# Performance work log

Measured on AMD Instinct MI355X. Metric: run time of the kernel, lower is better.

The kernel has to match this reference:

```python
import jax, jax.numpy as jnp
import numpy as np

EPS = 1e-05
BITW = 8
BITA = 8


def _ste_round(v):
    # round with identity gradient (TF Round->Identity override)
    return v + jax.lax.stop_gradient(jnp.round(v) - v)


def _quantize_overflow(x, bits):
    # tensorlayer _quantize_overflow: linear quantization over [min, max]
    n = 2.0 ** bits - 1.0
    mx = jnp.max(x)
    mn = jnp.min(x)
    step = jax.lax.stop_gradient((mx - mn) / n)
    return _ste_round((x - mn) / step) * step + mn


def _conv2d_same(x, w):
    # x: [N,H,W,C], w: [KH,KW,C,F]
    return jax.lax.conv_general_dilated(
        x, w, window_strides=(1, 1), padding='SAME',
        dimension_numbers=('NHWC', 'HWIO', 'NHWC'))


def setup_inputs() -> dict:
    key = jax.random.key(0)
    k1, k2 = jax.random.split(key)
    x = jax.random.normal(k1, (32, 56, 56, 128), dtype=jnp.float32)
    W = jax.random.normal(k2, (3, 3, 128, 256), dtype=jnp.float32) * 0.02
    gamma = jnp.ones((256,), dtype=jnp.float32)
    beta = jnp.zeros((256,), dtype=jnp.float32)
    return {"x": x, "W": W, "gamma": gamma, "beta": beta}


def reference(x, W, gamma, beta):
    # 1) fake-quantize activations
    xq = _quantize_overflow(x, BITA)
    # 2) full-precision conv to get batch statistics (training path)
    conv_out = _conv2d_same(x, W)  # [N,H,W,F]
    mean = jnp.mean(conv_out, axis=(0, 1, 2))          # [F]
    var = jnp.var(conv_out, axis=(0, 1, 2))            # [F], biased (tf.nn.moments)
    inv_std = 1.0 / jnp.sqrt(var + EPS)                # [F]
    # 3) fold BN into weights/bias
    w_fold = W * (gamma * inv_std)                     # broadcast over [KH,KW,C,F]
    bias_fold = beta - gamma * mean * inv_std          # [F]
    # 4) quantize folded weights, conv with quantized activations
    wq = _quantize_overflow(w_fold, BITW)
    out = _conv2d_same(xq, wq) + bias_fold
    return jax.nn.relu(out)
```

## Files before the change

kernel.cpp:

```cpp
#include <hip/hip_runtime.h>

typedef float f32x4_t __attribute__((ext_vector_type(4)));
typedef __bf16 bf16x8_t __attribute__((ext_vector_type(8)));
typedef unsigned short u16x8_t __attribute__((ext_vector_type(8)));

#define NPIX        100352
#define PIX_PER_IMG 3136
#define PH          58
#define PPIX        3364
#define C_IN        128
#define C_OUT       256
#define NTAPS       9
#define NV4         3211264
#define NWELEM      294912
#define MBLK        784
#define NPADPIX     107648

#define OFF_ENC     0
#define OFF_WQP     16
#define OFF_XQP     32
#define OFF_SCALE   64
#define OFF_BIAS    1152
#define OFF_WT      4096
#define OFF_WQT     593920
#define OFF_PSUM    1183744
#define OFF_PSQ     1986560
#define OFF_XPAD    2789376
#define OFF_XQPAD   30347264

__device__ __forceinline__ unsigned short f2bf(float x) {
  unsigned u = __float_as_uint(x);
  u += 0x7FFFu + ((u >> 16) & 1u);
  return (unsigned short)(u >> 16);
}
__device__ __forceinline__ unsigned encf(float v) {
  unsigned u = __float_as_uint(v);
  return (u & 0x80000000u) ? ~u : (u | 0x80000000u);
}
__device__ __forceinline__ float decf(unsigned e) {
  unsigned u = (e & 0x80000000u) ? (e ^ 0x80000000u) : ~e;
  return __uint_as_float(u);
}
__device__ __forceinline__ void gl_lds16(const void* g, void* l) {
  auto gp = (const __attribute__((address_space(1))) unsigned*)(const unsigned*)g;
  auto lp = (__attribute__((address_space(3))) unsigned*)(unsigned*)l;
  __builtin_amdgcn_global_load_lds(gp, lp, 16, 0, 0);
}

__global__ void kinit(unsigned* enc) {
  enc[0] = 0xFFFFFFFFu;
  enc[1] = 0u;
  enc[2] = 0xFFFFFFFFu;
  enc[3] = 0u;
}

__global__ void kminmax(const float4* __restrict__ x, unsigned* __restrict__ enc) {
  const int tid = blockIdx.x * blockDim.x + threadIdx.x;
  const int stride = gridDim.x * blockDim.x;
  float mn = 3.4e38f, mx = -3.4e38f;
  for (int i = tid; i < NV4; i += stride) {
    float4 v = x[i];
    mn = fminf(mn, fminf(fminf(v.x, v.y), fminf(v.z, v.w)));
    mx = fmaxf(mx, fmaxf(fmaxf(v.x, v.y), fmaxf(v.z, v.w)));
  }
  #pragma unroll
  for (int off = 32; off > 0; off >>= 1) {
    mn = fminf(mn, __shfl_xor(mn, off));
    mx = fmaxf(mx, __shfl_xor(mx, off));
  }
  __shared__ float smn[4], smx[4];
  const int lane = threadIdx.x & 63, w = threadIdx.x >> 6;
  if (lane == 0) { smn[w] = mn; smx[w] = mx; }
  __syncthreads();
  if (threadIdx.x == 0) {
    mn = fminf(fminf(smn[0], smn[1]), fminf(smn[2], smn[3]));
    mx = fmaxf(fmaxf(smx[0], smx[1]), fmaxf(smx[2], smx[3]));
    atomicMin(&enc[0], encf(mn));
    atomicMax(&enc[1], encf(mx));
  }
}

__global__ void kprep(const unsigned* __restrict__ enc, float* __restrict__ xqp) {
  const float mn = decf(enc[0]), mx = decf(enc[1]);
  xqp[0] = mn;
  xqp[1] = (mx - mn) / 255.0f;
  xqp[2] = 255.0f / (mx - mn);
}

__global__ void kwconv(const float* __restrict__ W, unsigned short* __restrict__ wt) {
  const int idx = blockIdx.x * 256 + threadIdx.x;
  if (idx >= NWELEM) return;
  const int c = idx & 127;
  const int f = (idx >> 7) & 255;
  const int tap = idx >> 15;
  wt[idx] = f2bf(W[(tap * 128 + c) * 256 + f]);
}

__global__ void kwq(const float* __restrict__ W, const float* __restrict__ scale,
                    const float* __restrict__ wqp, unsigned short* __restrict__ wqt) {
  const int idx = blockIdx.x * 256 + threadIdx.x;
  if (idx >= NWELEM) return;
  const int c = idx & 127;
  const int f = (idx >> 7) & 255;
  const int tap = idx >> 15;
  const float wmn = wqp[0], wstep = wqp[1], wrstep = wqp[2];
  const float v = W[(tap * 128 + c) * 256 + f] * scale[f];
  const float q = rintf((v - wmn) * wrstep) * wstep + wmn;
  wqt[idx] = f2bf(q);
}

__global__ void kpadfill(const float* __restrict__ x, const float* __restrict__ xqp,
                         unsigned short* __restrict__ xpad, unsigned short* __restrict__ xqpad)
{
  const int tid = blockIdx.x * 256 + threadIdx.x;
  if (tid >= NPADPIX * 16) return;
  const int pp = tid >> 4;
  const int c8 = (tid & 15) << 3;
  const int n = pp / PPIX;
  const int rem = pp - n * PPIX;
  const int hp = rem / PH;
  const int wp = rem - hp * PH;
  u16x8_t vb, vq;
  #pragma unroll
  for (int j = 0; j < 8; ++j) { vb[j] = 0; vq[j] = 0; }
  if (hp >= 1 && hp <= 56 && wp >= 1 && wp <= 56) {
    const float mn = xqp[0], step = xqp[1], rstep = xqp[2];
    const float* src = x + ((n * PIX_PER_IMG) + (hp - 1) * 56 + (wp - 1)) * C_IN + c8;
    const float4 a = *(const float4*)src;
    const float4 b = *(const float4*)(src + 4);
    const float v[8] = {a.x, a.y, a.z, a.w, b.x, b.y, b.z, b.w};
    #pragma unroll
    for (int j = 0; j < 8; ++j) {
      vb[j] = f2bf(v[j]);
      const float qv = rintf((v[j] - mn) * rstep) * step + mn;
      vq[j] = f2bf(qv);
    }
  }
  *(u16x8_t*)(xpad + pp * C_IN + c8) = vb;
  *(u16x8_t*)(xqpad + pp * C_IN + c8) = vq;
}

template<int STATS>
__global__ __launch_bounds__(512, 4)
void kconv(const unsigned short* __restrict__ xin,
           const unsigned short* __restrict__ wt,
           float* __restrict__ out,
           const float* __restrict__ bias,
           float* __restrict__ psum,
           float* __restrict__ psq)
{
  const int bm = blockIdx.x;
  const int bn = blockIdx.y;
  const int tid = threadIdx.x;
  const int lane = tid & 63;
  const int wid = tid >> 6;
  const int wm = wid >> 2;
  const int wn = wid & 3;
  const int l16 = lane & 15;
  const int rsub = lane >> 4;

  __shared__ __align__(16) unsigned char smem[65536];
  unsigned char* smA = smem;
  unsigned char* smB = smem + 32768;

  const int rbase = wid * 4 + rsub;
  const int gchunk = (l16 & 8) | ((l16 & 7) ^ (rbase & 7));

  unsigned aoff[4];
  #pragma unroll
  for (int i = 0; i < 4; ++i) {
    const int pix = bm * 128 + i * 32 + rbase;
    const int n = pix / PIX_PER_IMG;
    const int rem = pix - n * PIX_PER_IMG;
    const int h = rem / 56;
    const int w = rem - h * 56;
    aoff[i] = (unsigned)((n * PPIX + h * PH + w) * C_IN + gchunk * 8);
  }
  unsigned boff[4];
  #pragma unroll
  for (int i = 0; i < 4; ++i) {
    const int f = bn * 128 + i * 32 + rbase;
    boff[i] = (unsigned)(f * C_IN + gchunk * 8);
  }

  f32x4_t acc[4][2];
  #pragma unroll
  for (int im = 0; im < 4; ++im)
    #pragma unroll
    for (int in = 0; in < 2; ++in)
      #pragma unroll
      for (int k = 0; k < 4; ++k) acc[im][in][k] = 0.f;

  #pragma unroll 1
  for (int tap = 0; tap < NTAPS; ++tap) {
    const int kh = tap / 3, kw = tap - kh * 3;
    const unsigned atap = (unsigned)((kh * PH + kw) * C_IN);
    const unsigned btap = (unsigned)(tap * C_OUT * C_IN);
    __syncthreads();
    #pragma unroll
    for (int i = 0; i < 4; ++i)
      gl_lds16(xin + atap + aoff[i], smA + i * 8192 + wid * 1024);
    #pragma unroll
    for (int i = 0; i < 4; ++i)
      gl_lds16(wt + btap + boff[i], smB + i * 8192 + wid * 1024);
    __syncthreads();

    #pragma unroll
    for (int kb = 0; kb < 4; ++kb) {
      bf16x8_t av[4], bv[2];
      const int c = kb * 4 + rsub;
      const int p = (c & 8) | ((c & 7) ^ (l16 & 7));
      #pragma unroll
      for (int im = 0; im < 4; ++im) {
        const int row = wm * 64 + im * 16 + l16;
        av[im] = *(const bf16x8_t*)(smA + row * 256 + p * 16);
      }
      #pragma unroll
      for (int in = 0; in < 2; ++in) {
        const int row = wn * 32 + in * 16 + l16;
        bv[in] = *(const bf16x8_t*)(smB + row * 256 + p * 16);
      }
      #pragma unroll
      for (int im = 0; im < 4; ++im)
        #pragma unroll
        for (int in = 0; in < 2; ++in)
          acc[im][in] = __builtin_amdgcn_mfma_f32_16x16x32_bf16(av[im], bv[in], acc[im][in], 0, 0, 0);
    }
  }

  if (STATS) {
    __syncthreads();
    float* sb = (float*)smem;
    #pragma unroll
    for (int in = 0; in < 2; ++in) {
      float s = 0.f, q = 0.f;
      #pragma unroll
      for (int im = 0; im < 4; ++im)
        #pragma unroll
        for (int j = 0; j < 4; ++j) {
          const float v = acc[im][in][j];
          s += v; q += v * v;
        }
      s += __shfl_xor(s, 16); q += __shfl_xor(q, 16);
      s += __shfl_xor(s, 32); q += __shfl_xor(q, 32);
      if (lane < 16) {
        sb[wid * 32 + in * 16 + lane] = s;
        sb[256 + wid * 32 + in * 16 + lane] = q;
      }
    }
    __syncthreads();
    if (tid < 128) {
      const int wn2 = tid >> 5, cw = tid & 31;
      const float s = sb[wn2 * 32 + cw] + sb[(4 + wn2) * 32 + cw];
      const float q = sb[256 + wn2 * 32 + cw] + sb[256 + (4 + wn2) * 32 + cw];
      const int b = bm * 2 + bn;
      psum[b * 128 + tid] = s;
      psq[b * 128 + tid] = q;
    }
  } else {
    float bval[2];
    #pragma unroll
    for (int in = 0; in < 2; ++in)
      bval[in] = bias[bn * 128 + wn * 32 + in * 16 + l16];
    #pragma unroll
    for (int im = 0; im < 4; ++im) {
      #pragma unroll
      for (int j = 0; j < 4; ++j) {
        const int pix = bm * 128 + wm * 64 + im * 16 + rsub * 4 + j;
        #pragma unroll
        for (int in = 0; in < 2; ++in) {
          const int f = bn * 128 + wn * 32 + in * 16 + l16;
          out[pix * 256 + f] = fmaxf(acc[im][in][j] + bval[in], 0.f);
        }
      }
    }
  }
}

__global__ __launch_bounds__(256)
void kstats(const float* __restrict__ psum, const float* __restrict__ psq,
            const float* __restrict__ gamma, const float* __restrict__ beta,
            float* __restrict__ scale, float* __restrict__ bias)
{
  const int ch = blockIdx.x;
  const int bn = ch >> 7, col = ch & 127;
  float s = 0.f, q = 0.f;
  for (int bm = threadIdx.x; bm < MBLK; bm += 256) {
    const int b = bm * 2 + bn;
    s += psum[b * 128 + col];
    q += psq[b * 128 + col];
  }
  #pragma unroll
  for (int off = 32; off > 0; off >>= 1) {
    s += __shfl_xor(s, off);
    q += __shfl_xor(q, off);
  }
  __shared__ float ss[4], sq2[4];
  const int lane = threadIdx.x & 63, w = threadIdx.x >> 6;
  if (lane == 0) { ss[w] = s; sq2[w] = q; }
  __syncthreads();
  if (threadIdx.x == 0) {
    s = ss[0] + ss[1] + ss[2] + ss[3];
    q = sq2[0] + sq2[1] + sq2[2] + sq2[3];
    const float inv = 1.0f / (float)NPIX;
    const float mean = s * inv;
    const float var = q * inv - mean * mean;
    const float istd = 1.0f / sqrtf(var + 1e-5f);
    const float g = gamma[ch];
    scale[ch] = g * istd;
    bias[ch] = beta[ch] - g * mean * istd;
  }
}

__global__ __launch_bounds__(256)
void kwmm(const float* __restrict__ W, const float* __restrict__ scale,
          unsigned* __restrict__ enc)
{
  const int idx = blockIdx.x * 256 + threadIdx.x;
  float v = 0.f;
  if (idx < NWELEM) v = W[idx] * scale[idx & 255];
  float mn = v, mx = v;
  #pragma unroll
  for (int off = 32; off > 0; off >>= 1) {
    mn = fminf(mn, __shfl_xor(mn, off));
    mx = fmaxf(mx, __shfl_xor(mx, off));
  }
  __shared__ float rmn[4], rmx[4];
  const int lane = threadIdx.x & 63, w = threadIdx.x >> 6;
  if (lane == 0) { rmn[w] = mn; rmx[w] = mx; }
  __syncthreads();
  if (threadIdx.x == 0) {
    mn = fminf(fminf(rmn[0], rmn[1]), fminf(rmn[2], rmn[3]));
    mx = fmaxf(fmaxf(rmx[0], rmx[1]), fmaxf(rmx[2], rmx[3]));
    atomicMin(&enc[2], encf(mn));
    atomicMax(&enc[3], encf(mx));
  }
}

__global__ void kwprep(const unsigned* __restrict__ enc, float* __restrict__ wqp) {
  const float mn = decf(enc[2]), mx = decf(enc[3]);
  wqp[0] = mn;
  wqp[1] = (mx - mn) / 255.0f;
  wqp[2] = 255.0f / (mx - mn);
}

extern "C" void kernel_launch(void* const* d_in, const int* in_sizes, int n_in,
                              void* d_out, int out_size, void* d_ws, size_t ws_size,
                              hipStream_t stream)
{
  const float* x     = (const float*)d_in[0];
  const float* W     = (const float*)d_in[1];
  const float* gamma = (const float*)d_in[2];
  const float* beta  = (const float*)d_in[3];
  float* out = (float*)d_out;
  char* ws = (char*)d_ws;

  unsigned* enc        = (unsigned*)(ws + OFF_ENC);
  float* wqp           = (float*)(ws + OFF_WQP);
  float* xqp           = (float*)(ws + OFF_XQP);
  float* scale         = (float*)(ws + OFF_SCALE);
  float* bias          = (float*)(ws + OFF_BIAS);
  unsigned short* Wt   = (unsigned short*)(ws + OFF_WT);
  unsigned short* Wqt  = (unsigned short*)(ws + OFF_WQT);
  float* psum          = (float*)(ws + OFF_PSUM);
  float* psq           = (float*)(ws + OFF_PSQ);
  unsigned short* xpad  = (unsigned short*)(ws + OFF_XPAD);
  unsigned short* xqpad = (unsigned short*)(ws + OFF_XQPAD);

  kinit<<<1, 64, 0, stream>>>(enc);
  kminmax<<<1024, 256, 0, stream>>>((const float4*)x, enc);
  kprep<<<1, 64, 0, stream>>>(enc, xqp);
  kwconv<<<1152, 256, 0, stream>>>(W, Wt);
  kpadfill<<<6728, 256, 0, stream>>>(x, xqp, xpad, xqpad);
  kconv<1><<<dim3(MBLK, 2), 512, 0, stream>>>(xpad, Wt, nullptr, nullptr, psum, psq);
  kstats<<<256, 256, 0, stream>>>(psum, psq, gamma, beta, scale, bias);
  kwmm<<<1152, 256, 0, stream>>>(W, scale, enc);
  kwprep<<<1, 64, 0, stream>>>(enc, wqp);
  kwq<<<1152, 256, 0, stream>>>(W, scale, wqp, Wqt);
  kconv<0><<<dim3(MBLK, 2), 512, 0, stream>>>(xqpad, Wqt, out, bias, nullptr, nullptr);
}
```

Baseline: 257.9 us.

## Enlarge conv tiles to 256x128, double-buffer half-tap K stages, remap blocks per XCD

The implicit-GEMM conv kernel now computes 256-pixel by 128-filter tiles per block, with each warp holding a 64x64 accumulator (16 MFMA tiles). The K loop is split into 18 half-tap stages of 64 channels and double-buffered in 96KB of LDS, so the next stage's global-to-LDS load overlaps the MFMAs of the current one. Blocks are remapped so that each XCD gets a contiguous range of pixel tiles, which should improve L2 reuse. In exchange, register and LDS pressure rise (launch bounds drop to 2 blocks per CU), and the stats partials are indexed for the new tile shape.

```diff
diff --git a/kernel.cpp b/kernel.cpp
--- a/kernel.cpp
+++ b/kernel.cpp
@@ -13,7 +13,7 @@
 #define NTAPS       9
 #define NV4         3211264
 #define NWELEM      294912
-#define MBLK        784
+#define MBLK2       392
 #define NPADPIX     107648
 
 #define OFF_ENC     0
@@ -141,7 +141,7 @@
 }
 
 template<int STATS>
-__global__ __launch_bounds__(512, 4)
+__global__ __launch_bounds__(512, 2)
 void kconv(const unsigned short* __restrict__ xin,
            const unsigned short* __restrict__ wt,
            float* __restrict__ out,
@@ -149,90 +149,97 @@
            float* __restrict__ psum,
            float* __restrict__ psq)
 {
-  const int bm = blockIdx.x;
-  const int bn = blockIdx.y;
+  const int l = blockIdx.x;
+  const int xcd = l & 7, k = l >> 3;
+  const int bn = k & 1;
+  const int bm = xcd * 49 + (k >> 1);
+
   const int tid = threadIdx.x;
   const int lane = tid & 63;
   const int wid = tid >> 6;
-  const int wm = wid >> 2;
-  const int wn = wid & 3;
+  const int wm = wid >> 1;
+  const int wn = wid & 1;
   const int l16 = lane & 15;
   const int rsub = lane >> 4;
 
-  __shared__ __align__(16) unsigned char smem[65536];
-  unsigned char* smA = smem;
-  unsigned char* smB = smem + 32768;
-
-  const int rbase = wid * 4 + rsub;
-  const int gchunk = (l16 & 8) | ((l16 & 7) ^ (rbase & 7));
-
+  __shared__ __align__(16) unsigned char smem[98304];
+
+  const int lrow = lane >> 3;
+  const int lchunk = (lane & 7) ^ lrow;
   unsigned aoff[4];
   #pragma unroll
-  for (int i = 0; i < 4; ++i) {
-    const int pix = bm * 128 + i * 32 + rbase;
+  for (int r = 0; r < 4; ++r) {
+    const int pix = bm * 256 + r * 64 + wid * 8 + lrow;
     const int n = pix / PIX_PER_IMG;
     const int rem = pix - n * PIX_PER_IMG;
-    const int h = rem / 56;
-    const int w = rem - h * 56;
-    aoff[i] = (unsigned)((n * PPIX + h * PH + w) * C_IN + gchunk * 8);
-  }
-  unsigned boff[4];
-  #pragma unroll
-  for (int i = 0; i < 4; ++i) {
-    const int f = bn * 128 + i * 32 + rbase;
-    boff[i] = (unsigned)(f * C_IN + gchunk * 8);
-  }
-
-  f32x4_t acc[4][2];
+    const int hh = rem / 56;
+    const int ww = rem - hh * 56;
+    aoff[r] = (unsigned)((n * PPIX + hh * PH + ww) * C_IN + lchunk * 8);
+  }
+  unsigned boff[2];
+  #pragma unroll
+  for (int r = 0; r < 2; ++r) {
+    const int f = bn * 128 + r * 64 + wid * 8 + lrow;
+    boff[r] = (unsigned)(f * C_IN + lchunk * 8);
+  }
+
+  f32x4_t acc[4][4];
   #pragma unroll
   for (int im = 0; im < 4; ++im)
     #pragma unroll
-    for (int in = 0; in < 2; ++in)
-      #pragma unroll
-      for (int k = 0; k < 4; ++k) acc[im][in][k] = 0.f;
+    for (int in = 0; in < 4; ++in)
+      #pragma unroll
+      for (int j = 0; j < 4; ++j) acc[im][in][j] = 0.f;
+
+  auto stage = [&](int bsel, int s) {
+    const int tap = s >> 1, h = (s & 1) << 6;
+    const int kh = tap / 3, kw = tap - kh * 3;
+    const unsigned atap = (unsigned)((kh * PH + kw) * C_IN + h);
+    const unsigned btap = (unsigned)(tap * C_OUT * C_IN + h);
+    unsigned char* sA = smem + bsel * 49152;
+    unsigned char* sB = sA + 32768;
+    #pragma unroll
+    for (int r = 0; r < 4; ++r)
+      gl_lds16(xin + atap + aoff[r], sA + r * 8192 + wid * 1024);
+    #pragma unroll
+    for (int r = 0; r < 2; ++r)
+      gl_lds16(wt + btap + boff[r], sB + r * 8192 + wid * 1024);
+  };
+
+  stage(0, 0);
+  __syncthreads();
+  int cur = 0;
 
   #pragma unroll 1
-  for (int tap = 0; tap < NTAPS; ++tap) {
-    const int kh = tap / 3, kw = tap - kh * 3;
-    const unsigned atap = (unsigned)((kh * PH + kw) * C_IN);
-    const unsigned btap = (unsigned)(tap * C_OUT * C_IN);
-    __syncthreads();
-    #pragma unroll
-    for (int i = 0; i < 4; ++i)
-      gl_lds16(xin + atap + aoff[i], smA + i * 8192 + wid * 1024);
-    #pragma unroll
-    for (int i = 0; i < 4; ++i)
-      gl_lds16(wt + btap + boff[i], smB + i * 8192 + wid * 1024);
-    __syncthreads();
-
-    #pragma unroll
-    for (int kb = 0; kb < 4; ++kb) {
-      bf16x8_t av[4], bv[2];
+  for (int s = 0; s < 18; ++s) {
+    if (s < 17) stage(cur ^ 1, s + 1);
+    const unsigned char* sA = smem + cur * 49152;
+    const unsigned char* sB = sA + 32768;
+    #pragma unroll
+    for (int kb = 0; kb < 2; ++kb) {
       const int c = kb * 4 + rsub;
-      const int p = (c & 8) | ((c & 7) ^ (l16 & 7));
-      #pragma unroll
-      for (int im = 0; im < 4; ++im) {
-        const int row = wm * 64 + im * 16 + l16;
-        av[im] = *(const bf16x8_t*)(smA + row * 256 + p * 16);
-      }
-      #pragma unroll
-      for (int in = 0; in < 2; ++in) {
-        const int row = wn * 32 + in * 16 + l16;
-        bv[in] = *(const bf16x8_t*)(smB + row * 256 + p * 16);
-      }
+      const int p = c ^ (l16 & 7);
+      bf16x8_t av[4], bv[4];
+      #pragma unroll
+      for (int im = 0; im < 4; ++im)
+        av[im] = *(const bf16x8_t*)(sA + (wm * 64 + im * 16 + l16) * 128 + p * 16);
+      #pragma unroll
+      for (int in = 0; in < 4; ++in)
+        bv[in] = *(const bf16x8_t*)(sB + (wn * 64 + in * 16 + l16) * 128 + p * 16);
       #pragma unroll
       for (int im = 0; im < 4; ++im)
         #pragma unroll
-        for (int in = 0; in < 2; ++in)
+        for (int in = 0; in < 4; ++in)
           acc[im][in] = __builtin_amdgcn_mfma_f32_16x16x32_bf16(av[im], bv[in], acc[im][in], 0, 0, 0);
     }
+    __syncthreads();
+    cur ^= 1;
   }
 
   if (STATS) {
-    __syncthreads();
     float* sb = (float*)smem;
     #pragma unroll
-    for (int in = 0; in < 2; ++in) {
+    for (int in = 0; in < 4; ++in) {
       float s = 0.f, q = 0.f;
       #pragma unroll
       for (int im = 0; im < 4; ++im)
@@ -244,32 +251,36 @@
       s += __shfl_xor(s, 16); q += __shfl_xor(q, 16);
       s += __shfl_xor(s, 32); q += __shfl_xor(q, 32);
       if (lane < 16) {
-        sb[wid * 32 + in * 16 + lane] = s;
-        sb[256 + wid * 32 + in * 16 + lane] = q;
+        sb[wid * 64 + in * 16 + lane] = s;
+        sb[512 + wid * 64 + in * 16 + lane] = q;
       }
     }
     __syncthreads();
     if (tid < 128) {
-      const int wn2 = tid >> 5, cw = tid & 31;
-      const float s = sb[wn2 * 32 + cw] + sb[(4 + wn2) * 32 + cw];
-      const float q = sb[256 + wn2 * 32 + cw] + sb[256 + (4 + wn2) * 32 + cw];
+      const int wn2 = tid >> 6, cl = tid & 63;
+      float s = 0.f, q = 0.f;
+      #pragma unroll
+      for (int wm2 = 0; wm2 < 4; ++wm2) {
+        s += sb[(wm2 * 2 + wn2) * 64 + cl];
+        q += sb[512 + (wm2 * 2 + wn2) * 64 + cl];
+      }
       const int b = bm * 2 + bn;
       psum[b * 128 + tid] = s;
       psq[b * 128 + tid] = q;
     }
   } else {
-    float bval[2];
-    #pragma unroll
-    for (int in = 0; in < 2; ++in)
-      bval[in] = bias[bn * 128 + wn * 32 + in * 16 + l16];
+    float bval[4];
+    #pragma unroll
+    for (int in = 0; in < 4; ++in)
+      bval[in] = bias[bn * 128 + wn * 64 + in * 16 + l16];
     #pragma unroll
     for (int im = 0; im < 4; ++im) {
       #pragma unroll
       for (int j = 0; j < 4; ++j) {
-        const int pix = bm * 128 + wm * 64 + im * 16 + rsub * 4 + j;
+        const int pix = bm * 256 + wm * 64 + im * 16 + rsub * 4 + j;
         #pragma unroll
-        for (int in = 0; in < 2; ++in) {
-          const int f = bn * 128 + wn * 32 + in * 16 + l16;
+        for (int in = 0; in < 4; ++in) {
+          const int f = bn * 128 + wn * 64 + in * 16 + l16;
           out[pix * 256 + f] = fmaxf(acc[im][in][j] + bval[in], 0.f);
         }
       }
@@ -285,7 +296,7 @@
   const int ch = blockIdx.x;
   const int bn = ch >> 7, col = ch & 127;
   float s = 0.f, q = 0.f;
-  for (int bm = threadIdx.x; bm < MBLK; bm += 256) {
+  for (int bm = threadIdx.x; bm < MBLK2; bm += 256) {
     const int b = bm * 2 + bn;
     s += psum[b * 128 + col];
     q += psq[b * 128 + col];
@@ -372,10 +383,10 @@
   kprep<<<1, 64, 0, stream>>>(enc, xqp);
   kwconv<<<1152, 256, 0, stream>>>(W, Wt);
   kpadfill<<<6728, 256, 0, stream>>>(x, xqp, xpad, xqpad);
-  kconv<1><<<dim3(MBLK, 2), 512, 0, stream>>>(xpad, Wt, nullptr, nullptr, psum, psq);
+  kconv<1><<<784, 512, 0, stream>>>(xpad, Wt, nullptr, nullptr, psum, psq);
   kstats<<<256, 256, 0, stream>>>(psum, psq, gamma, beta, scale, bias);
   kwmm<<<1152, 256, 0, stream>>>(W, scale, enc);
   kwprep<<<1, 64, 0, stream>>>(enc, wqp);
   kwq<<<1152, 256, 0, stream>>>(W, scale, wqp, Wqt);
-  kconv<0><<<dim3(MBLK, 2), 512, 0, stream>>>(xqpad, Wqt, out, bias, nullptr, nullptr);
-}
+  kconv<0><<<784, 512, 0, stream>>>(xqpad, Wqt, out, bias, nullptr, nullptr);
+}
```

Measured after the change: 243.5 us. -5.6%, faster.
